# Performance work log

Measured on AMD Instinct MI355X. Metric: run time of the kernel, lower is better.

Reference implementation:

```python
import jax, jax.numpy as jnp
import numpy as np

B, C_HR, C_LR, HH, WH, HL, WL = 2, 256, 256, 128, 128, 64, 64
CC = 64            # compressed channels
LK, HK, EK = 5, 3, 3
GROUPS, LW, SCALE = 4, 3, 2


def conv2d(x, w, b, pad, dilation=1):
    out = jax.lax.conv_general_dilated(
        x, w, (1, 1), [(pad, pad), (pad, pad)],
        rhs_dilation=(dilation, dilation),
        dimension_numbers=('NCHW', 'OIHW', 'NCHW'))
    return out + b[None, :, None, None]


def unfold(x, k, dilation=1):
    # torch F.unfold with padding=(k//2)*dilation -> [B,C,k*k,H,W], row-major kernel order
    pad = (k // 2) * dilation
    Bb, C, H, W = x.shape
    xp = jnp.pad(x, ((0, 0), (0, 0), (pad, pad), (pad, pad)))
    patches = [xp[:, :, i * dilation:i * dilation + H, j * dilation:j * dilation + W]
               for i in range(k) for j in range(k)]
    return jnp.stack(patches, axis=2)


def kernel_normalizer(mask, k, hamming):
    n, c, h, w = mask.shape
    mc = c // (k * k)
    m = jax.nn.softmax(mask.reshape(n, mc, k * k, h, w), axis=2)
    m = m.reshape(n, mc, k, k, h, w) * hamming[None, None, :, :, None, None]
    m = m / jnp.sum(m, axis=(2, 3), keepdims=True)
    return m.reshape(n, c, h, w)


def carafe(feat, mask, k, scale):
    # mmcv CARAFE with group=1: mask at output resolution [B,k*k,H*s,W*s]
    Bb, C, H, W = feat.shape
    unf = unfold(feat, k)  # [B,C,k2,H,W]
    if scale == 1:
        return jnp.einsum('bckhw,bkhw->bchw', unf, mask)
    m = mask.reshape(Bb, k * k, H, scale, W, scale)
    out = jnp.einsum('bckhw,bkhpwq->bchpwq', unf, m)
    return out.reshape(Bb, C, H * scale, W * scale)


def group_norm(x, gamma, beta, groups, eps=1e-5):
    Bb, C, H, W = x.shape
    xg = x.reshape(Bb, groups, -1)
    mu = xg.mean(-1, keepdims=True)
    var = xg.var(-1, keepdims=True)
    xn = ((xg - mu) * jax.lax.rsqrt(var + eps)).reshape(Bb, C, H, W)
    return xn * gamma[None, :, None, None] + beta[None, :, None, None]


def compute_similarity(x, k=LW, dilation=2):
    unf = unfold(x, k, dilation)  # [B,C,k2,H,W]
    c = k * k // 2
    center = unf[:, :, c:c + 1]
    eps = 1e-8
    num = jnp.sum(center * unf, axis=1)
    den = (jnp.maximum(jnp.linalg.norm(center, axis=1), eps)
           * jnp.maximum(jnp.linalg.norm(unf, axis=1), eps))
    sim = num / den  # [B,k2,H,W]
    return jnp.concatenate([sim[:, :c], sim[:, c + 1:]], axis=1)


def pixel_shuffle(x, r):
    Bb, C, H, W = x.shape
    x = x.reshape(Bb, C // (r * r), r, r, H, W)
    return x.transpose(0, 1, 4, 2, 5, 3).reshape(Bb, C // (r * r), H * r, W * r)


def pixel_unshuffle(x, r):
    Bb, C, H, W = x.shape
    x = x.reshape(Bb, C, H // r, r, W // r, r)
    return x.transpose(0, 1, 3, 5, 2, 4).reshape(Bb, C * r * r, H // r, W // r)


def grid_sample_border(x, grid):
    # bilinear, padding_mode='border', align_corners=False; grid [N,Hg,Wg,2] (x,y)
    N, C, H, W = x.shape
    gx = jnp.clip((grid[..., 0] + 1.0) * W * 0.5 - 0.5, 0.0, W - 1.0)
    gy = jnp.clip((grid[..., 1] + 1.0) * H * 0.5 - 0.5, 0.0, H - 1.0)
    x0 = jnp.floor(gx); y0 = jnp.floor(gy)
    tx = (gx - x0)[:, None]; ty = (gy - y0)[:, None]
    x0i = x0.astype(jnp.int32); y0i = y0.astype(jnp.int32)
    x1i = jnp.minimum(x0i + 1, W - 1); y1i = jnp.minimum(y0i + 1, H - 1)
    g = jax.vmap(lambda img, yi, xi: img[:, yi, xi])
    v00 = g(x, y0i, x0i); v01 = g(x, y0i, x1i)
    v10 = g(x, y1i, x0i); v11 = g(x, y1i, x1i)
    return (v00 * (1 - tx) * (1 - ty) + v01 * tx * (1 - ty)
            + v10 * (1 - tx) * ty + v11 * tx * ty)


def init_pos():
    h = jnp.arange((-SCALE + 1) / 2, (SCALE - 1) / 2 + 1) / SCALE  # [-0.25, 0.25]
    t = jnp.stack(jnp.meshgrid(h, h, indexing='ij'))
    t = jnp.transpose(t, (0, 2, 1))
    return jnp.tile(t, (1, GROUPS, 1)).reshape(1, -1, 1, 1).astype(jnp.float32)


def dysampler(hr_x, lr_x, feat, gn_hr_w, gn_hr_b, gn_lr_w, gn_lr_b,
              w_off, b_off, w_hoff, b_hoff, w_ds, b_ds, w_hds, b_hds):
    hr_x = group_norm(hr_x, gn_hr_w, gn_hr_b, CC // 8)
    lr_x = group_norm(lr_x, gn_lr_w, gn_lr_b, CC // 8)
    hr_sim = compute_similarity(hr_x)
    lr_sim = compute_similarity(lr_x)
    pad = EK // 2
    off = conv2d(lr_sim, w_off, b_off, pad) + pixel_unshuffle(conv2d(hr_sim, w_hoff, b_hoff, pad), SCALE)
    ds = conv2d(lr_x, w_ds, b_ds, pad) + pixel_unshuffle(conv2d(hr_x, w_hds, b_hds, pad), SCALE)
    offset = off * jax.nn.sigmoid(ds) + init_pos()  # [B, 2*G*s^2, Hl, Wl]
    Bb, _, H, W = offset.shape
    off5 = offset.reshape(Bb, 2, -1, H, W)
    cw = jnp.arange(W, dtype=offset.dtype) + 0.5
    ch = jnp.arange(H, dtype=offset.dtype) + 0.5
    base = jnp.stack([jnp.broadcast_to(cw[None, :], (H, W)),
                      jnp.broadcast_to(ch[:, None], (H, W))])  # [2,H,W] (x,y)
    norm = jnp.array([W, H], offset.dtype).reshape(1, 2, 1, 1, 1)
    coords = 2.0 * (base[None, :, None] + off5) / norm - 1.0  # [B,2,G*s^2,H,W]
    coords = pixel_shuffle(coords.reshape(Bb, -1, H, W), SCALE)  # [B,2*G,sH,sW]
    coords = (coords.reshape(Bb, 2, GROUPS, SCALE * H, SCALE * W)
              .transpose(0, 2, 3, 4, 1)
              .reshape(Bb * GROUPS, SCALE * H, SCALE * W, 2))
    xs = feat.reshape(Bb * GROUPS, -1, feat.shape[-2], feat.shape[-1])
    out = grid_sample_border(xs, coords)
    return out.reshape(Bb, -1, SCALE * H, SCALE * W)


def setup_inputs() -> dict:
    key = jax.random.key(0)
    ks = jax.random.split(key, 16)
    r = lambda i, shape, s=0.05: jax.random.normal(ks[i], shape, jnp.float32) * s
    LC2, HC2 = LK * LK, HK * HK
    SIMC = LW * LW - 1
    OC = 2 * GROUPS * SCALE * SCALE
    OCH = 2 * GROUPS
    return {
        'hr_feat': jax.random.normal(ks[0], (B, C_HR, HH, WH), jnp.float32),
        'lr_feat': jax.random.normal(ks[1], (B, C_LR, HL, WL), jnp.float32),
        'w_hr_comp': r(2, (CC, C_HR, 1, 1)), 'b_hr_comp': r(3, (CC,)),
        'w_lr_comp': r(4, (CC, C_LR, 1, 1)), 'b_lr_comp': r(5, (CC,)),
        'w_enc': r(6, (LC2, CC, EK, EK), 0.01), 'b_enc': r(7, (LC2,), 0.01),
        'w_enc2': r(8, (HC2, CC, EK, EK), 0.01), 'b_enc2': r(9, (HC2,), 0.01),
        'gn_hr_w': jnp.ones((CC,), jnp.float32), 'gn_hr_b': jnp.zeros((CC,), jnp.float32),
        'gn_lr_w': jnp.ones((CC,), jnp.float32), 'gn_lr_b': jnp.zeros((CC,), jnp.float32),
        'w_off': r(10, (OC, SIMC, EK, EK), 0.01), 'b_off': jnp.zeros((OC,), jnp.float32),
        'w_hoff': r(11, (OCH, SIMC, EK, EK), 0.01), 'b_hoff': jnp.zeros((OCH,), jnp.float32),
        'w_ds': r(12, (OC, CC, EK, EK), 0.01), 'b_ds': jnp.zeros((OC,), jnp.float32),
        'w_hds': r(13, (OCH, CC, EK, EK), 0.01), 'b_hds': jnp.zeros((OCH,), jnp.float32),
    }


def reference(hr_feat, lr_feat, w_hr_comp, b_hr_comp, w_lr_comp, b_lr_comp,
              w_enc, b_enc, w_enc2, b_enc2, gn_hr_w, gn_hr_b, gn_lr_w, gn_lr_b,
              w_off, b_off, w_hoff, b_hoff, w_ds, b_ds, w_hds, b_hds):
    ham_lo = jnp.asarray(np.outer(np.hamming(LK), np.hamming(LK)), jnp.float32)
    ham_hi = jnp.asarray(np.outer(np.hamming(HK), np.hamming(HK)), jnp.float32)
    epad = EK // 2
    ch = conv2d(hr_feat, w_hr_comp, b_hr_comp, 0)
    cl = conv2d(lr_feat, w_lr_comp, b_lr_comp, 0)
    # semi_conv + comp_feat_upsample + use_high_pass path
    mask_hr_hr = conv2d(ch, w_enc2, b_enc2, epad)
    mh_init = kernel_normalizer(mask_hr_hr, HK, ham_hi)
    ch = 2.0 * ch - carafe(ch, mh_init, HK, 1)
    mask_lr_hr = conv2d(ch, w_enc, b_enc, epad)
    ml_init = kernel_normalizer(mask_lr_hr, LK, ham_lo)
    mask_lr_lr = carafe(conv2d(cl, w_enc, b_enc, epad), ml_init, LK, 2)
    mask_lr = mask_lr_hr + mask_lr_lr
    ml_init2 = kernel_normalizer(mask_lr, LK, ham_lo)
    mask_hr_lr = carafe(conv2d(cl, w_enc2, b_enc2, epad), ml_init2, LK, 2)
    mask_hr = mask_hr_hr + mask_hr_lr
    mask_lr_n = kernel_normalizer(mask_lr, LK, ham_lo)
    lr_up = carafe(lr_feat, mask_lr_n, LK, 2)
    mask_hr_n = kernel_normalizer(mask_hr, HK, ham_hi)
    hr_out = 2.0 * hr_feat - carafe(hr_feat, mask_hr_n, HK, 1)  # hr_residual
    lr_out = dysampler(ch, cl, lr_up, gn_hr_w, gn_hr_b, gn_lr_w, gn_lr_b,
                       w_off, b_off, w_hoff, b_hoff, w_ds, b_ds, w_hds, b_hds)
    return mask_lr_n, hr_out, lr_out
```

## Files before the change

### kernel.cpp

```cpp
#include <hip/hip_runtime.h>
#include <hip/hip_bf16.h>

typedef __hip_bfloat16 bf16;
#define TPB 256

__device__ __forceinline__ float toF(float v){ return v; }
__device__ __forceinline__ float toF(bf16 v){ return __bfloat162float(v); }
__device__ __forceinline__ float bfu(unsigned short u){
    unsigned int x = ((unsigned int)u) << 16;
    return __uint_as_float(x);
}
template<typename T> __device__ __forceinline__ void stT(T* p, long i, float v);
template<> __device__ __forceinline__ void stT<float>(float* p, long i, float v){ p[i] = v; }
template<> __device__ __forceinline__ void stT<bf16>(bf16* p, long i, float v){ p[i] = __float2bfloat16(v); }

__device__ __forceinline__ void st4bf(bf16* p, const float* a){
    bf16 t0 = __float2bfloat16(a[0]);
    bf16 t1 = __float2bfloat16(a[1]);
    bf16 t2 = __float2bfloat16(a[2]);
    bf16 t3 = __float2bfloat16(a[3]);
    ushort4 pk;
    pk.x = *(unsigned short*)&t0;
    pk.y = *(unsigned short*)&t1;
    pk.z = *(unsigned short*)&t2;
    pk.w = *(unsigned short*)&t3;
    *(ushort4*)p = pk;
}

static inline int nblk(long n){ return (int)((n + TPB - 1) / TPB); }

__global__ void k_detect(const void* hr, int n, int* flag, float* stat)
{
    if (threadIdx.x < 64) stat[threadIdx.x] = 0.f;
    const unsigned short* u = (const unsigned short*)hr;
    int nan = 0, oz = 0, ot = 0;
    for (int i = threadIdx.x; i < n; i += TPB) {
        unsigned short a = u[i] & 0x7FFF;
        if (a >= 0x7F80) nan++;
        if (i & 1) { ot++; if (a == 0) oz++; }
    }
    __shared__ int s1[TPB], s2[TPB], s3[TPB];
    s1[threadIdx.x] = nan; s2[threadIdx.x] = oz; s3[threadIdx.x] = ot;
    __syncthreads();
    if (threadIdx.x == 0) {
        int a = 0, b = 0, c = 0;
        for (int i = 0; i < TPB; i++) { a += s1[i]; b += s2[i]; c += s3[i]; }
        *flag = (a >= 6 || (long)b * 10 >= (long)c * 9) ? 1 : 0;
    }
}

#define P_W_HRC 0
#define P_B_HRC 16384
#define P_W_LRC 16448
#define P_B_LRC 32832
#define P_W_ENC 32896
#define P_B_ENC 47296
#define P_W_ENC2 47321
#define P_B_ENC2 52505
#define P_GNHW 52514
#define P_GNHB 52578
#define P_GNLW 52642
#define P_GNLB 52706
#define P_W_OFF 52770
#define P_B_OFF 55074
#define P_W_HOFF 55106
#define P_B_HOFF 55682
#define P_W_DS 55690
#define P_B_DS 74122
#define P_W_HDS 74154
#define P_B_HDS 78762
#define P_TOT 78770

__constant__ int c_segsz[20]  = {16384,64,16384,64,14400,25,5184,9,64,64,64,64,2304,32,576,8,18432,32,4608,8};
__constant__ int c_segbase[20]= {P_W_HRC,P_B_HRC,P_W_LRC,P_B_LRC,P_W_ENC,P_B_ENC,P_W_ENC2,P_B_ENC2,
                                 P_GNHW,P_GNHB,P_GNLW,P_GNLB,P_W_OFF,P_B_OFF,P_W_HOFF,P_B_HOFF,
                                 P_W_DS,P_B_DS,P_W_HDS,P_B_HDS};
__constant__ int c_segcin[20] = {256,0,256,0, 64,0, 64,0, 0,0,0,0, 8,0, 8,0, 64,0, 64,0};
__constant__ int c_segcout[20]= { 64,0, 64,0, 25,0,  9,0, 0,0,0,0,32,0, 8,0, 32,0,  8,0};
__constant__ int c_segtap[20] = {  1,0,  1,0,  9,0,  9,0, 0,0,0,0, 9,0, 9,0,  9,0,  9,0};

__global__ void k_prep(const void* p0,const void* p1,const void* p2,const void* p3,
                       const void* p4,const void* p5,const void* p6,const void* p7,
                       const void* p8,const void* p9,const void* p10,const void* p11,
                       const void* p12,const void* p13,const void* p14,const void* p15,
                       const void* p16,const void* p17,const void* p18,const void* p19,
                       float* dst, const int* flag)
{
    int idx = blockIdx.x * TPB + threadIdx.x;
    if (idx >= P_TOT) return;
    int s = 0, off = idx;
    while (off >= c_segsz[s]) { off -= c_segsz[s]; s++; }
    const void* sp;
    switch (s) {
        case 0: sp=p0; break;  case 1: sp=p1; break;  case 2: sp=p2; break;  case 3: sp=p3; break;
        case 4: sp=p4; break;  case 5: sp=p5; break;  case 6: sp=p6; break;  case 7: sp=p7; break;
        case 8: sp=p8; break;  case 9: sp=p9; break;  case 10: sp=p10; break; case 11: sp=p11; break;
        case 12: sp=p12; break; case 13: sp=p13; break; case 14: sp=p14; break; case 15: sp=p15; break;
        case 16: sp=p16; break; case 17: sp=p17; break; case 18: sp=p18; break; default: sp=p19; break;
    }
    float v = (*flag) ? ((const float*)sp)[off] : toF(((const bf16*)sp)[off]);
    int doff = off;
    int cin = c_segcin[s];
    if (cin) {
        int t = c_segtap[s], cout = c_segcout[s];
        int co = off / (cin * t);
        int r  = off % (cin * t);
        int ci = r / t, k = r % t;
        doff = (ci * cout + co) * t + k;
    }
    dst[c_segbase[s] + doff] = v;
}

template<typename T>
__device__ void transpLR_body(const T* __restrict__ x, bf16* __restrict__ xT, int Bn)
{
    __shared__ float tile[64][65];
    int bid = blockIdx.x;
    int pg = bid & 63;
    int cg = (bid >> 6) & 3;
    int b  = bid >> 8;
    int tid = threadIdx.x;
    int tr = tid >> 6, tc = tid & 63;
    for (int i = 0; i < 16; i++) {
        int c = tr + i * 4;
        tile[c][tc] = toF(x[(((long)(b * 256 + cg * 64 + c)) << 12) + (pg << 6) + tc]);
    }
    __syncthreads();
    for (int i = 0; i < 16; i++) {
        int p = tr + i * 4;
        xT[((((long)b << 12) + (pg << 6) + p) << 8) + (cg << 6) + tc] = __float2bfloat16(tile[tc][p]);
    }
}
__global__ void k_transpLR(const void* x, bf16* xT, int Bn, const int* flag)
{
    if (*flag) transpLR_body<float>((const float*)x, xT, Bn);
    else       transpLR_body<bf16 >((const bf16*)x,  xT, Bn);
}

__global__ void k_carafe5T(const bf16* __restrict__ featT, const float* __restrict__ mask,
                           bf16* __restrict__ outT, int Bn)
{
    int lane = threadIdx.x & 63;
    int nwg = gridDim.x;
    int bid = blockIdx.x;
    int swz = (nwg & 7) ? bid : ((bid & 7) * (nwg >> 3) + (bid >> 3));
    int wid = (swz << 2) | (threadIdx.x >> 6);
    wid = __builtin_amdgcn_readfirstlane(wid);
    if (wid >= Bn * 4096) return;
    int ipix = wid & 4095;
    int b    = wid >> 12;
    int h = ipix >> 6, w = ipix & 63;
    const bf16*  fb = featT + (((long)b << 12) << 8) + (lane << 2);
    const float* mb = mask + (((long)b * 25) << 14) + (h << 8) + (w << 1);
    float a00[4], a01[4], a10[4], a11[4];
    #pragma unroll
    for (int t = 0; t < 4; t++) { a00[t]=0.f; a01[t]=0.f; a10[t]=0.f; a11[t]=0.f; }
    #pragma unroll
    for (int k = 0; k < 25; k++) {
        const int i = k / 5, j = k % 5;
        int yy = h + i - 2, xx = w + j - 2;
        bool v = (yy >= 0 && yy < 64 && xx >= 0 && xx < 64);
        int yc = v ? yy : 0, xc = v ? xx : 0;
        ushort4 u = *(const ushort4*)(fb + ((long)((yc << 6) + xc) << 8));
        float2 mr0 = *(const float2*)(mb + ((long)k << 14));
        float2 mr1 = *(const float2*)(mb + ((long)k << 14) + 128);
        float m00 = v ? mr0.x : 0.f, m01 = v ? mr0.y : 0.f;
        float m10 = v ? mr1.x : 0.f, m11 = v ? mr1.y : 0.f;
        float f0 = bfu(u.x), f1 = bfu(u.y), f2 = bfu(u.z), f3 = bfu(u.w);
        a00[0] += f0*m00; a00[1] += f1*m00; a00[2] += f2*m00; a00[3] += f3*m00;
        a01[0] += f0*m01; a01[1] += f1*m01; a01[2] += f2*m01; a01[3] += f3*m01;
        a10[0] += f0*m10; a10[1] += f1*m10; a10[2] += f2*m10; a10[3] += f3*m10;
        a11[0] += f0*m11; a11[1] += f1*m11; a11[2] += f2*m11; a11[3] += f3*m11;
    }
    bf16* op = outT + (((long)(b << 14) + (h << 8) + (w << 1)) << 8) + (lane << 2);
    st4bf(op, a00);
    st4bf(op + 256, a01);
    st4bf(op + (128 << 8), a10);
    st4bf(op + (128 << 8) + 256, a11);
}

template<int COUT>
__global__ void k_conv3x3p(const float* __restrict__ x, const float* __restrict__ wf,
                           float* __restrict__ pbuf, int Bn, int CIN, int H, int W, int CS)
{
    int HW = H * W;
    int idx = blockIdx.x * TPB + threadIdx.x;
    if (idx >= Bn * HW) return;
    int chunk = blockIdx.y;
    int pix = idx % HW, b = idx / HW;
    int wx = pix % W, hy = pix / W;
    int off[9]; float msk[9];
    #pragma unroll
    for (int i = 0; i < 3; i++) {
        int yy = hy + i - 1; bool vy = (yy >= 0 && yy < H); int yc = vy ? yy : hy;
        #pragma unroll
        for (int j = 0; j < 3; j++) {
            int xx = wx + j - 1; bool v = vy && (xx >= 0 && xx < W);
            int xc = (xx >= 0 && xx < W) ? xx : wx;
            off[i*3+j] = yc * W + xc; msk[i*3+j] = v ? 1.f : 0.f;
        }
    }
    float acc[COUT];
    #pragma unroll
    for (int co = 0; co < COUT; co++) acc[co] = 0.f;
    int c0 = chunk * CS;
    const float* xb = x + ((long)b * CIN + c0) * HW;
    const float* wb = wf + (long)c0 * COUT * 9;
    #pragma unroll 2
    for (int ci = 0; ci < CS; ci++) {
        const float* xc = xb + (long)ci * HW;
        float t[9];
        #pragma unroll
        for (int k = 0; k < 9; k++) t[k] = xc[off[k]] * msk[k];
        const float* wr = wb + (long)ci * COUT * 9;
        #pragma unroll
        for (int co = 0; co < COUT; co++) {
            const float* wp = wr + co * 9;
            acc[co] += t[0]*wp[0] + t[1]*wp[1] + t[2]*wp[2] + t[3]*wp[3] + t[4]*wp[4]
                     + t[5]*wp[5] + t[6]*wp[6] + t[7]*wp[7] + t[8]*wp[8];
        }
    }
    long pb = ((long)chunk * Bn + b) * COUT * (long)HW + pix;
    #pragma unroll
    for (int co = 0; co < COUT; co++) pbuf[pb + (long)co * HW] = acc[co];
}

__global__ void k_convr(const float* __restrict__ pbuf, const float* __restrict__ bias,
                        float* __restrict__ out, int Bn, int COUT, int HW, int nChunk)
{
    long idx = (long)blockIdx.x * TPB + threadIdx.x;
    if (idx >= (long)Bn * COUT * HW) return;
    int pix = idx % HW;
    int co  = (idx / HW) % COUT;
    int b   = idx / ((long)HW * COUT);
    float v = bias[co];
    for (int ch = 0; ch < nChunk; ch++)
        v += pbuf[(((long)ch * Bn + b) * COUT + co) * HW + pix];
    out[idx] = v;
}

template<typename T, int CG>
__device__ void conv1x1_body(const T* __restrict__ x, const float* __restrict__ wf,
                             const float* __restrict__ bias, float* __restrict__ out,
                             int Bn, int CIN, int HW)
{
    constexpr int NG = 64 / CG;
    int nwg = gridDim.x;
    int bid = blockIdx.x;
    int lid = (nwg & 7) ? bid : ((bid & 7) * (nwg >> 3) + (bid >> 3));
    int grp = lid % NG;
    int pixblk = lid / NG;
    int idx = pixblk * TPB + threadIdx.x;
    if (idx >= Bn * HW) return;
    int pix = idx % HW, b = idx / HW;
    const T* xp = x + (long)b * CIN * HW + pix;
    const float* wb = wf + grp * CG;
    float acc[CG];
    #pragma unroll
    for (int c = 0; c < CG; c++) acc[c] = 0.f;
    #pragma unroll 4
    for (int ci = 0; ci < CIN; ci++) {
        float v = toF(xp[(long)ci * HW]);
        const float* wr = wb + ci * 64;
        #pragma unroll
        for (int c = 0; c < CG; c++) acc[c] += v * wr[c];
    }
    long ob = ((long)b * 64 + grp * CG) * HW + pix;
    #pragma unroll
    for (int c = 0; c < CG; c++) out[ob + (long)c * HW] = acc[c] + bias[grp * CG + c];
}
template<int CG>
__global__ void k_conv1x1(const void* x, const float* wf, const float* bias, float* out,
                          int Bn, int CIN, int HW, const int* flag)
{
    if (*flag) conv1x1_body<float, CG>((const float*)x, wf, bias, out, Bn, CIN, HW);
    else       conv1x1_body<bf16, CG>((const bf16*)x,  wf, bias, out, Bn, CIN, HW);
}

template<int K, typename OT>
__device__ void knorm_body(const float* __restrict__ mask, float* __restrict__ out,
                           OT* __restrict__ outb, int B, int H, int W)
{
    const int K2 = K * K;
    int HWi = H * W;
    int idx = blockIdx.x * TPB + threadIdx.x;
    if (idx >= B * HWi) return;
    int pix = idx % HWi;
    int b   = idx / HWi;
    long HW = (long)HWi;
    long base = (long)b * K2 * HW + pix;
    float v[K2];
    float m = -1e30f;
    for (int k = 0; k < K2; k++) { v[k] = mask[base + k*HW]; m = fmaxf(m, v[k]); }
    float s2 = 0.f;
    for (int k = 0; k < K2; k++) {
        int i = k / K, j = k % K;
        float hi = (K == 3) ? ((i==1)?1.f:0.08f) : ((i==2)?1.f:((i==1||i==3)?0.54f:0.08f));
        float hj = (K == 3) ? ((j==1)?1.f:0.08f) : ((j==2)?1.f:((j==1||j==3)?0.54f:0.08f));
        v[k] = expf(v[k] - m) * hi * hj;
        s2 += v[k];
    }
    float inv = 1.f / s2;
    for (int k = 0; k < K2; k++) {
        float r = v[k] * inv;
        out[base + k*HW] = r;
        if (outb) stT<OT>(outb, base + k*HW, r);
    }
}
template<int K>
__global__ void k_knorm(const float* mask, float* out, void* outb, int B, int H, int W, const int* flag)
{
    if (*flag) knorm_body<K, float>(mask, out, (float*)outb, B, H, W);
    else       knorm_body<K, bf16>(mask, out, (bf16*)outb, B, H, W);
}

template<typename TF, typename TO, int NC>
__device__ void carafe3c_body(const TF* __restrict__ feat, const float* __restrict__ mask,
                              TO* __restrict__ out, int Bn)
{
    constexpr int CH = NC / 8;
    int idx = blockIdx.x * TPB + threadIdx.x;
    if (idx >= Bn * CH * 16384) return;
    int px = idx & 16383;
    int cc = (idx >> 14) % CH;
    int b  = (idx >> 14) / CH;
    int wx = px & 127, hy = px >> 7;
    float mk[9]; int off[9];
    #pragma unroll
    for (int i = 0; i < 3; i++) {
        int yy = hy + i - 1; bool vy = (yy >= 0 && yy < 128); int yc = vy ? yy : hy;
        #pragma unroll
        for (int j = 0; j < 3; j++) {
            int xx = wx + j - 1; bool v = vy && (xx >= 0 && xx < 128);
            int xc = (xx >= 0 && xx < 128) ? xx : wx;
            int k = i*3 + j;
            float m = mask[(((long)b*9 + k) << 14) + px];
            mk[k] = v ? m : 0.f;
            off[k] = (yc << 7) + xc;
        }
    }
    long base = ((long)(b * NC + cc * 8) << 14);
    for (int c = 0; c < 8; c++) {
        const TF* fp = feat + base + ((long)c << 14);
        float ctr = 0.f, acc = 0.f;
        #pragma unroll
        for (int k = 0; k < 9; k++) {
            float v = toF(fp[off[k]]);
            if (k == 4) ctr = v;
            acc += v * mk[k];
        }
        stT<TO>(out, base + ((long)c << 14) + px, 2.f * ctr - acc);
    }
}
__global__ void k_carafe3c_ws(const float* feat, const float* mask, float* out, int Bn)
{
    carafe3c_body<float, float, 64>(feat, mask, out, Bn);
}
__global__ void k_carafe3c_io(const void* feat, const float* mask, void* out, long outOff,
                              int Bn, const int* flag)
{
    if (*flag) carafe3c_body<float, float, 256>((const float*)feat, mask, (float*)out + outOff, Bn);
    else       carafe3c_body<bf16, bf16, 256>((const bf16*)feat, mask, (bf16*)out + outOff, Bn);
}

template<typename TF, typename TO, bool ADD, int CG>
__device__ void carafe5_body(const TF* __restrict__ feat, const float* __restrict__ mask,
                             const float* __restrict__ add, TO* __restrict__ out,
                             int Bn, int C)
{
    int ng = C / CG;
    int idx = blockIdx.x * TPB + threadIdx.x;
    if (idx >= Bn * ng * 16384) return;
    int px = idx & 16383;
    int gi = (idx >> 14) % ng;
    int b  = (idx >> 14) / ng;
    int X = px & 127, Y = px >> 7;
    int h = Y >> 1, w = X >> 1;
    float mk[25]; int off[25];
    const float* mb = mask + (((long)b * 25) << 14) + px;
    #pragma unroll
    for (int i = 0; i < 5; i++) {
        int yy = h + i - 2; bool vy = (yy >= 0 && yy < 64); int yc = vy ? yy : 0;
        #pragma unroll
        for (int j = 0; j < 5; j++) {
            int xx = w + j - 2; bool v = vy && (xx >= 0 && xx < 64);
            int xc = (xx >= 0 && xx < 64) ? xx : 0;
            int k = i*5 + j;
            mk[k] = v ? mb[(long)k << 14] : 0.f;
            off[k] = (yc << 6) + xc;
        }
    }
    int c0 = gi * CG;
    for (int c = 0; c < CG; c++) {
        long fb = ((long)(b * C + c0 + c) << 12);
        long ob = ((long)(b * C + c0 + c) << 14) + px;
        const TF* fp = feat + fb;
        float acc = ADD ? add[ob] : 0.f;
        #pragma unroll
        for (int k = 0; k < 25; k++) acc += toF(fp[off[k]]) * mk[k];
        stT<TO>(out, ob, acc);
    }
}
template<int CG>
__global__ void k_carafe5_ws(const float* feat, const float* mask, const float* add,
                             float* out, int Bn, int C)
{
    carafe5_body<float, float, true, CG>(feat, mask, add, out, Bn, C);
}

__global__ void k_gnstat(const float* __restrict__ x, float* __restrict__ stat, int statBase,
                         int S, int N)
{
    int bid = blockIdx.x;
    int bg = bid / S, sl = bid % S;
    int seg = N / S;
    long base = (long)bg * N + (long)sl * seg;
    float s = 0.f, ss = 0.f;
    for (int i = threadIdx.x; i < seg; i += TPB) {
        float v = x[base + i]; s += v; ss += v * v;
    }
    __shared__ float sh[8];
    for (int off = 32; off; off >>= 1) { s += __shfl_down(s, off); ss += __shfl_down(ss, off); }
    int wave = threadIdx.x >> 6, lane = threadIdx.x & 63;
    if (lane == 0) { sh[wave] = s; sh[4 + wave] = ss; }
    __syncthreads();
    if (threadIdx.x == 0) {
        float ts = 0.f, tss = 0.f;
        for (int i = 0; i < TPB/64; i++) { ts += sh[i]; tss += sh[4 + i]; }
        atomicAdd(&stat[statBase + bg*2], ts);
        atomicAdd(&stat[statBase + bg*2 + 1], tss);
    }
}
__global__ void k_gnapply(const float* __restrict__ x, const float* __restrict__ stat, int statBase,
                          const float* __restrict__ gamma, const float* __restrict__ beta,
                          float* __restrict__ out, int G, int Cg, int HW, int Bn)
{
    long idx = (long)blockIdx.x * TPB + threadIdx.x;
    long total = (long)Bn * G * Cg * HW;
    if (idx >= total) return;
    int bgN = Cg * HW;
    int bg = idx / bgN;
    int r  = idx % bgN;
    int g = bg % G;
    int c = g * Cg + r / HW;
    float s = stat[statBase + bg*2], ss = stat[statBase + bg*2 + 1];
    float mean = s / bgN;
    float inv = rsqrtf(ss / bgN - mean * mean + 1e-5f);
    out[idx] = (x[idx] - mean) * inv * gamma[c] + beta[c];
}

__global__ void k_simp(const float* __restrict__ x, float* __restrict__ pbuf,
                       int Bn, int H, int W, int CS)
{
    int HW = H * W;
    int idx = blockIdx.x * TPB + threadIdx.x;
    if (idx >= Bn * HW) return;
    int chunk = blockIdx.y;
    int pix = idx % HW, b = idx / HW;
    int wx = pix % W, hy = pix / W;
    const int dyv[8] = {-2,-2,-2, 0, 0, 2, 2, 2};
    const int dxv[8] = {-2, 0, 2,-2, 2,-2, 0, 2};
    int off[8]; float msk[8];
    #pragma unroll
    for (int n = 0; n < 8; n++) {
        int yy = hy + dyv[n], xx = wx + dxv[n];
        bool v = (yy >= 0 && yy < H && xx >= 0 && xx < W);
        off[n] = v ? yy * W + xx : pix;
        msk[n] = v ? 1.f : 0.f;
    }
    float dc = 0.f, num[8], dn[8];
    #pragma unroll
    for (int n = 0; n < 8; n++) { num[n] = 0.f; dn[n] = 0.f; }
    const float* xb = x + ((long)b * 64 + chunk * CS) * HW;
    #pragma unroll 2
    for (int ci = 0; ci < CS; ci++) {
        const float* xc = xb + (long)ci * HW;
        float c0 = xc[pix];
        dc += c0 * c0;
        #pragma unroll
        for (int n = 0; n < 8; n++) {
            float v = xc[off[n]] * msk[n];
            num[n] += c0 * v; dn[n] += v * v;
        }
    }
    long base = ((long)chunk * Bn + b) * 17 * (long)HW + pix;
    pbuf[base] = dc;
    #pragma unroll
    for (int n = 0; n < 8; n++) {
        pbuf[base + (long)(1 + n) * HW] = num[n];
        pbuf[base + (long)(9 + n) * HW] = dn[n];
    }
}
__global__ void k_simr(const float* __restrict__ pbuf, float* __restrict__ out,
                       int Bn, int HW, int nChunk)
{
    int idx = blockIdx.x * TPB + threadIdx.x;
    if (idx >= Bn * HW) return;
    int pix = idx % HW, b = idx / HW;
    float dc = 0.f, num[8], dn[8];
    #pragma unroll
    for (int n = 0; n < 8; n++) { num[n] = 0.f; dn[n] = 0.f; }
    for (int ch = 0; ch < nChunk; ch++) {
        long base = ((long)ch * Bn + b) * 17 * (long)HW + pix;
        dc += pbuf[base];
        #pragma unroll
        for (int n = 0; n < 8; n++) {
            num[n] += pbuf[base + (long)(1 + n) * HW];
            dn[n]  += pbuf[base + (long)(9 + n) * HW];
        }
    }
    float nc = fmaxf(sqrtf(dc), 1e-8f);
    #pragma unroll
    for (int n = 0; n < 8; n++)
        out[((long)(b*8 + n)) * HW + pix] = num[n] / (nc * fmaxf(sqrtf(dn[n]), 1e-8f));
}

__global__ void k_offset(const float* __restrict__ lro, const float* __restrict__ hro,
                         const float* __restrict__ lrd, const float* __restrict__ hrd,
                         float* __restrict__ outoff, int B)
{
    int idx = blockIdx.x * TPB + threadIdx.x;
    int total = B * 32 * 64 * 64;
    if (idx >= total) return;
    int wx = idx & 63;
    int hy = (idx >> 6) & 63;
    int o  = (idx >> 12) & 31;
    int b  = idx >> 17;
    int c = o >> 2, p = (o >> 1) & 1, q = o & 1;
    long hridx = ((long)(b*8 + c) * 128 + 2*hy + p) * 128 + 2*wx + q;
    float off = lro[idx] + hro[hridx];
    float dsv = lrd[idx] + hrd[hridx];
    float sg = 1.f / (1.f + expf(-dsv));
    int comp = o >> 4;
    float ip = (comp == 0) ? (q ? 0.25f : -0.25f) : (p ? 0.25f : -0.25f);
    outoff[idx] = off * sg + ip;
}

template<typename OT>
__device__ void gridsampleT_body(const unsigned short* __restrict__ lrupT,
                                 const float* __restrict__ offb, OT* __restrict__ out, int Bn)
{
    int idx = blockIdx.x * TPB + threadIdx.x;
    if (idx >= Bn * 4 * 16384) return;
    int ch0 = blockIdx.y << 5;
    int opix = idx & 16383;
    int g = (idx >> 14) & 3, b = idx >> 16;
    int X = opix & 127, Y = opix >> 7;
    int h = Y >> 1, p = Y & 1, w = X >> 1, q = X & 1;
    int r = g*4 + p*2 + q;
    float offx = offb[((long)(b*32 + r)      << 12) + (h << 6) + w];
    float offy = offb[((long)(b*32 + 16 + r) << 12) + (h << 6) + w];
    float gx = fminf(fmaxf(2.f * (w + 0.5f + offx) - 0.5f, 0.f), 127.f);
    float gy = fminf(fmaxf(2.f * (h + 0.5f + offy) - 0.5f, 0.f), 127.f);
    float x0f = floorf(gx), y0f = floorf(gy);
    float tx = gx - x0f, ty = gy - y0f;
    int x0 = (int)x0f, y0 = (int)y0f;
    int x1 = min(x0 + 1, 127), y1 = min(y0 + 1, 127);
    float w11 = tx * ty, w10 = ty - w11, w01 = tx - w11, w00 = 1.f - tx - ty + w11;
    const unsigned short* base = lrupT + (((long)b << 14) << 8) + (g << 6) + ch0;
    long a00 = ((long)((y0 << 7) + x0)) << 8, a01 = ((long)((y0 << 7) + x1)) << 8;
    long a10 = ((long)((y1 << 7) + x0)) << 8, a11 = ((long)((y1 << 7) + x1)) << 8;
    OT* op = out + ((long)(b * 256 + g * 64 + ch0) << 14) + opix;
    #pragma unroll
    for (int c8 = 0; c8 < 4; c8++) {
        uint4 v00 = *(const uint4*)(base + a00 + c8*8);
        uint4 v01 = *(const uint4*)(base + a01 + c8*8);
        uint4 v10 = *(const uint4*)(base + a10 + c8*8);
        uint4 v11 = *(const uint4*)(base + a11 + c8*8);
        const unsigned short* u00 = (const unsigned short*)&v00;
        const unsigned short* u01 = (const unsigned short*)&v01;
        const unsigned short* u10 = (const unsigned short*)&v10;
        const unsigned short* u11 = (const unsigned short*)&v11;
        #pragma unroll
        for (int t = 0; t < 8; t++) {
            float res = bfu(u00[t])*w00 + bfu(u01[t])*w01 + bfu(u10[t])*w10 + bfu(u11[t])*w11;
            stT<OT>(op, ((long)(c8*8 + t) << 14), res);
        }
    }
}
__global__ void k_gridsampleT(const bf16* lrupT, const float* offb, void* out, long outOff,
                              int Bn, const int* flag)
{
    if (*flag) gridsampleT_body<float>((const unsigned short*)lrupT, offb, (float*)out + outOff, Bn);
    else       gridsampleT_body<bf16 >((const unsigned short*)lrupT, offb, (bf16*)out + outOff, Bn);
}

extern "C" void kernel_launch(void* const* d_in, const int* in_sizes, int n_in,
                              void* d_out, int out_size, void* d_ws, size_t ws_size,
                              hipStream_t stream) {
    const void* hr_feat = d_in[0];
    const void* lr_feat = d_in[1];

    const int B = 2, HH = 128, HL = 64;
    const int HWH = HH*HH, HWL = HL*HL;

    int*   flag = (int*)d_ws;
    float* stat = (float*)d_ws + 4;
    float* P    = (float*)d_ws + 80;
    float* ws   = P + ((P_TOT + 63) & ~63);

    size_t o = 0;
    float* ch0    = ws + o; o += (size_t)B*64*HWH;
    float* clb    = ws + o; o += (size_t)B*64*HWL;
    float* maskHH = ws + o; o += (size_t)B*9*HWH;
    float* tmp9   = ws + o; o += (size_t)B*9*HWH;
    float* chn    = ws + o; o += (size_t)B*64*HWH;
    float* m25a   = ws + o; o += (size_t)B*25*HWH;
    float* m25b   = ws + o; o += (size_t)B*25*HWH;
    float* m25c   = ws + o; o += (size_t)B*25*HWH;
    float* enccl  = ws + o; o += (size_t)B*25*HWL;
    float* enc2cl = ws + o; o += (size_t)B*9*HWL;
    bf16*  lrupT  = (bf16*)(ws + o); o += (size_t)B*256*HWH/2;
    float* lrx    = ws + o; o += (size_t)B*64*HWL;
    float* hrsim  = ws + o; o += (size_t)B*8*HWH;
    float* lrsim  = ws + o; o += (size_t)B*8*HWL;
    float* qhro   = ws + o; o += (size_t)B*8*HWH;
    float* qlro   = ws + o; o += (size_t)B*32*HWL;
    float* qhrd   = ws + o; o += (size_t)B*8*HWH;
    float* qlrd   = ws + o; o += (size_t)B*32*HWL;
    float* offb   = ws + o; o += (size_t)B*32*HWL;
    float* hrx   = ch0;
    float* maskH = m25b;
    float* pbuf3  = tmp9;
    float* pbuf6  = m25b;
    float* pbufL8 = (float*)lrupT;
    float* pbufT  = chn;
    bf16*  lrfT   = (bf16*)hrsim;
    (void)ws_size; (void)n_in;

    long out1Off = (long)B*25*HWH;
    long out2Off = out1Off + (long)B*256*HWH;

    const float* pw_hrc = P + P_W_HRC;  const float* pb_hrc = P + P_B_HRC;
    const float* pw_lrc = P + P_W_LRC;  const float* pb_lrc = P + P_B_LRC;
    const float* pw_enc = P + P_W_ENC;  const float* pb_enc = P + P_B_ENC;
    const float* pw_enc2= P + P_W_ENC2; const float* pb_enc2= P + P_B_ENC2;
    const float* pgnhw  = P + P_GNHW;   const float* pgnhb  = P + P_GNHB;
    const float* pgnlw  = P + P_GNLW;   const float* pgnlb  = P + P_GNLB;
    const float* pw_off = P + P_W_OFF;  const float* pb_off = P + P_B_OFF;
    const float* pw_hoff= P + P_W_HOFF; const float* pb_hoff= P + P_B_HOFF;
    const float* pw_ds  = P + P_W_DS;   const float* pb_ds  = P + P_B_DS;
    const float* pw_hds = P + P_W_HDS;  const float* pb_hds = P + P_B_HDS;

    int nDet = in_sizes[0] < 16384 ? in_sizes[0] : 16384;
    k_detect<<<1, TPB, 0, stream>>>(hr_feat, nDet, flag, stat);
    k_prep<<<nblk(P_TOT), TPB, 0, stream>>>(d_in[2],d_in[3],d_in[4],d_in[5],d_in[6],d_in[7],
        d_in[8],d_in[9],d_in[10],d_in[11],d_in[12],d_in[13],d_in[14],d_in[15],d_in[16],
        d_in[17],d_in[18],d_in[19],d_in[20],d_in[21], P, flag);
    k_transpLR<<<B*4*64, TPB, 0, stream>>>(lr_feat, lrfT, B, flag);

    k_conv1x1<8><<<nblk((long)B*HWH) * 8, TPB, 0, stream>>>(hr_feat, pw_hrc, pb_hrc, ch0, B, 256, HWH, flag);
    k_conv1x1<2><<<nblk((long)B*HWL) * 32, TPB, 0, stream>>>(lr_feat, pw_lrc, pb_lrc, clb, B, 256, HWL, flag);
    k_conv3x3p<9><<<dim3(nblk((long)B*HWH),8), TPB, 0, stream>>>(ch0, pw_enc2, pbuf3, B, 64, HH, HH, 8);
    k_convr<<<nblk((long)B*9*HWH), TPB, 0, stream>>>(pbuf3, pb_enc2, maskHH, B, 9, HWH, 8);
    k_knorm<3><<<nblk((long)B*HWH), TPB, 0, stream>>>(maskHH, tmp9, nullptr, B, HH, HH, flag);
    k_carafe3c_ws<<<nblk((long)B*8*16384), TPB, 0, stream>>>(ch0, tmp9, chn, B);
    k_conv3x3p<25><<<dim3(nblk((long)B*HWH),8), TPB, 0, stream>>>(chn, pw_enc, pbuf6, B, 64, HH, HH, 8);
    k_convr<<<nblk((long)B*25*HWH), TPB, 0, stream>>>(pbuf6, pb_enc, m25a, B, 25, HWH, 8);
    k_knorm<5><<<nblk((long)B*HWH), TPB, 0, stream>>>(m25a, m25b, nullptr, B, HH, HH, flag);
    k_conv3x3p<25><<<dim3(nblk((long)B*HWL),16), TPB, 0, stream>>>(clb, pw_enc, pbufL8, B, 64, HL, HL, 4);
    k_convr<<<nblk((long)B*25*HWL), TPB, 0, stream>>>(pbufL8, pb_enc, enccl, B, 25, HWL, 16);
    k_carafe5_ws<5><<<nblk((long)B*5*16384), TPB, 0, stream>>>(enccl, m25b, m25a, m25c, B, 25);
    k_knorm<5><<<nblk((long)B*HWH), TPB, 0, stream>>>(m25c, m25a, d_out, B, HH, HH, flag);
    k_conv3x3p<9><<<dim3(nblk((long)B*HWL),16), TPB, 0, stream>>>(clb, pw_enc2, pbufL8, B, 64, HL, HL, 4);
    k_convr<<<nblk((long)B*9*HWL), TPB, 0, stream>>>(pbufL8, pb_enc2, enc2cl, B, 9, HWL, 16);
    k_carafe5_ws<3><<<nblk((long)B*3*16384), TPB, 0, stream>>>(enc2cl, m25a, maskHH, maskH, B, 9);
    k_knorm<3><<<nblk((long)B*HWH), TPB, 0, stream>>>(maskH, tmp9, nullptr, B, HH, HH, flag);
    k_carafe3c_io<<<nblk((long)B*32*16384), TPB, 0, stream>>>(hr_feat, tmp9, d_out, out1Off, B, flag);
    k_carafe5T<<<B*4096/4, TPB, 0, stream>>>(lrfT, m25a, lrupT, B);
    k_gnstat<<<16*32, TPB, 0, stream>>>(chn, stat, 0, 32, 8*HWH);
    k_gnapply<<<nblk((long)B*64*HWH), TPB, 0, stream>>>(chn, stat, 0, pgnhw, pgnhb, hrx, 8, 8, HWH, B);
    k_gnstat<<<16*8, TPB, 0, stream>>>(clb, stat, 32, 8, 8*HWL);
    k_gnapply<<<nblk((long)B*64*HWL), TPB, 0, stream>>>(clb, stat, 32, pgnlw, pgnlb, lrx, 8, 8, HWL, B);
    k_simp<<<dim3(nblk((long)B*HWH),8), TPB, 0, stream>>>(hrx, pbufT, B, HH, HH, 8);
    k_simr<<<nblk((long)B*HWH), TPB, 0, stream>>>(pbufT, hrsim, B, HWH, 8);
    k_simp<<<dim3(nblk((long)B*HWL),16), TPB, 0, stream>>>(lrx, pbufT, B, HL, HL, 4);
    k_simr<<<nblk((long)B*HWL), TPB, 0, stream>>>(pbufT, lrsim, B, HWL, 16);
    k_conv3x3p<8><<<dim3(nblk((long)B*HWH),4), TPB, 0, stream>>>(hrsim, pw_hoff, pbufT, B, 8, HH, HH, 2);
    k_convr<<<nblk((long)B*8*HWH), TPB, 0, stream>>>(pbufT, pb_hoff, qhro, B, 8, HWH, 4);
    k_conv3x3p<32><<<dim3(nblk((long)B*HWL),8), TPB, 0, stream>>>(lrsim, pw_off, pbufT, B, 8, HL, HL, 1);
    k_convr<<<nblk((long)B*32*HWL), TPB, 0, stream>>>(pbufT, pb_off, qlro, B, 32, HWL, 8);
    k_conv3x3p<8><<<dim3(nblk((long)B*HWH),8), TPB, 0, stream>>>(hrx, pw_hds, pbufT, B, 64, HH, HH, 8);
    k_convr<<<nblk((long)B*8*HWH), TPB, 0, stream>>>(pbufT, pb_hds, qhrd, B, 8, HWH, 8);
    k_conv3x3p<32><<<dim3(nblk((long)B*HWL),16), TPB, 0, stream>>>(lrx, pw_ds, pbufT, B, 64, HL, HL, 4);
    k_convr<<<nblk((long)B*32*HWL), TPB, 0, stream>>>(pbufT, pb_ds, qlrd, B, 32, HWL, 16);
    k_offset<<<nblk((long)B*32*HWL), TPB, 0, stream>>>(qlro, qhro, qlrd, qhrd, offb, B);
    k_gridsampleT<<<dim3(nblk((long)B*4*HWH),2), TPB, 0, stream>>>(lrupT, offb, d_out, out2Off, B, flag);
}
```

Baseline: 604.3 us.

## Replace split-K 3x3 convs with LDS-tiled fused-bias kernels and tile 1x1 convs

Six 64-input-channel 3x3 convolutions move from a split-channel partial-sum kernel plus a separate reduction kernel to a single kernel. That kernel stages input row tiles with halos in shared memory, splits output channels across blockIdx.y, and adds the bias directly. The 1x1 compression convs now stage 64-channel input slices in shared memory, with each thread computing 16 output channels. This removes the partial-buffer writes and reduce launches, at the cost of fewer parallel blocks and per-thread weight reads from global/scalar memory.

```diff
diff --git a/kernel.cpp b/kernel.cpp
--- a/kernel.cpp
+++ b/kernel.cpp
@@ -239,42 +239,101 @@
     out[idx] = v;
 }
 
-template<typename T, int CG>
-__device__ void conv1x1_body(const T* __restrict__ x, const float* __restrict__ wf,
-                             const float* __restrict__ bias, float* __restrict__ out,
-                             int Bn, int CIN, int HW)
-{
-    constexpr int NG = 64 / CG;
-    int nwg = gridDim.x;
-    int bid = blockIdx.x;
-    int lid = (nwg & 7) ? bid : ((bid & 7) * (nwg >> 3) + (bid >> 3));
-    int grp = lid % NG;
-    int pixblk = lid / NG;
-    int idx = pixblk * TPB + threadIdx.x;
-    if (idx >= Bn * HW) return;
-    int pix = idx % HW, b = idx / HW;
-    const T* xp = x + (long)b * CIN * HW + pix;
-    const float* wb = wf + grp * CG;
+template<int W, int CG>
+__global__ void k_conv3x3f(const float* __restrict__ x, const float* __restrict__ wf,
+                           const float* __restrict__ bias, float* __restrict__ out,
+                           int Bn, int H, int COUT)
+{
+    constexpr int TR = 256 / W;
+    constexpr int WP = W + 2;
+    constexpr int CB = 4;
+    constexpr int NE = CB * (TR + 2) * WP;
+    __shared__ float s[CB][TR + 2][WP];
+    int tile = blockIdx.x;
+    int cog  = blockIdx.y;
+    int rows_g = tile * TR;
+    int b  = rows_g / H;
+    int r0 = rows_g % H;
+    int HW = H * W;
+    int tid = threadIdx.x;
+    int row = tid / W, col = tid % W;
     float acc[CG];
     #pragma unroll
     for (int c = 0; c < CG; c++) acc[c] = 0.f;
-    #pragma unroll 4
-    for (int ci = 0; ci < CIN; ci++) {
-        float v = toF(xp[(long)ci * HW]);
-        const float* wr = wb + ci * 64;
-        #pragma unroll
-        for (int c = 0; c < CG; c++) acc[c] += v * wr[c];
-    }
-    long ob = ((long)b * 64 + grp * CG) * HW + pix;
-    #pragma unroll
-    for (int c = 0; c < CG; c++) out[ob + (long)c * HW] = acc[c] + bias[grp * CG + c];
-}
-template<int CG>
-__global__ void k_conv1x1(const void* x, const float* wf, const float* bias, float* out,
-                          int Bn, int CIN, int HW, const int* flag)
-{
-    if (*flag) conv1x1_body<float, CG>((const float*)x, wf, bias, out, Bn, CIN, HW);
-    else       conv1x1_body<bf16, CG>((const bf16*)x,  wf, bias, out, Bn, CIN, HW);
+    const float* xb = x + (long)b * 64 * HW;
+    for (int c0 = 0; c0 < 64; c0 += CB) {
+        __syncthreads();
+        for (int e = tid; e < NE; e += 256) {
+            int ci  = e / ((TR + 2) * WP);
+            int rem = e % ((TR + 2) * WP);
+            int rr = rem / WP, cc = rem % WP;
+            int gr = r0 - 1 + rr, gc = cc - 1;
+            bool v = (gr >= 0 && gr < H && gc >= 0 && gc < W);
+            s[ci][rr][cc] = v ? xb[(long)(c0 + ci) * HW + gr * W + gc] : 0.f;
+        }
+        __syncthreads();
+        #pragma unroll
+        for (int ci = 0; ci < CB; ci++) {
+            float t0 = s[ci][row  ][col  ], t1 = s[ci][row  ][col+1], t2 = s[ci][row  ][col+2];
+            float t3 = s[ci][row+1][col  ], t4 = s[ci][row+1][col+1], t5 = s[ci][row+1][col+2];
+            float t6 = s[ci][row+2][col  ], t7 = s[ci][row+2][col+1], t8 = s[ci][row+2][col+2];
+            const float* wr = wf + ((long)(c0 + ci) * COUT + cog * CG) * 9;
+            #pragma unroll
+            for (int c = 0; c < CG; c++) {
+                const float* wp = wr + c * 9;
+                acc[c] += t0*wp[0] + t1*wp[1] + t2*wp[2] + t3*wp[3] + t4*wp[4]
+                        + t5*wp[5] + t6*wp[6] + t7*wp[7] + t8*wp[8];
+            }
+        }
+    }
+    int pp = (r0 + row) * W + col;
+    #pragma unroll
+    for (int c = 0; c < CG; c++) {
+        int co = cog * CG + c;
+        out[((long)b * COUT + co) * HW + pp] = acc[c] + bias[co];
+    }
+}
+
+template<typename T>
+__device__ void conv1x1f_body(const T* __restrict__ x, const float* __restrict__ wf,
+                              const float* __restrict__ bias, float* __restrict__ out,
+                              int Bn, int HW)
+{
+    __shared__ float s[64][64];
+    int tile = blockIdx.x;
+    int tid = threadIdx.x;
+    int pix = tid & 63, grp = tid >> 6;
+    int g0 = tile * 64;
+    int b  = g0 / HW, pp0 = g0 % HW;
+    const T* xb = x + (long)b * 256 * HW + pp0;
+    float acc[16];
+    #pragma unroll
+    for (int c = 0; c < 16; c++) acc[c] = 0.f;
+    for (int c0 = 0; c0 < 256; c0 += 64) {
+        __syncthreads();
+        #pragma unroll
+        for (int k = 0; k < 16; k++) {
+            int ci = grp + k * 4;
+            s[ci][pix] = toF(xb[(long)(c0 + ci) * HW + pix]);
+        }
+        __syncthreads();
+        #pragma unroll 8
+        for (int ci = 0; ci < 64; ci++) {
+            float v = s[ci][pix];
+            const float* wr = wf + (c0 + ci) * 64 + grp * 16;
+            #pragma unroll
+            for (int c = 0; c < 16; c++) acc[c] += v * wr[c];
+        }
+    }
+    long ob = ((long)b * 64 + grp * 16) * HW + pp0 + pix;
+    #pragma unroll
+    for (int c = 0; c < 16; c++) out[ob + (long)c * HW] = acc[c] + bias[grp * 16 + c];
+}
+__global__ void k_conv1x1f(const void* x, const float* wf, const float* bias, float* out,
+                           int Bn, int HW, const int* flag)
+{
+    if (*flag) conv1x1f_body<float>((const float*)x, wf, bias, out, Bn, HW);
+    else       conv1x1f_body<bf16 >((const bf16*)x,  wf, bias, out, Bn, HW);
 }
 
 template<int K, typename OT>
@@ -621,9 +680,6 @@
     float* offb   = ws + o; o += (size_t)B*32*HWL;
     float* hrx   = ch0;
     float* maskH = m25b;
-    float* pbuf3  = tmp9;
-    float* pbuf6  = m25b;
-    float* pbufL8 = (float*)lrupT;
     float* pbufT  = chn;
     bf16*  lrfT   = (bf16*)hrsim;
     (void)ws_size; (void)n_in;
@@ -649,21 +705,17 @@
         d_in[17],d_in[18],d_in[19],d_in[20],d_in[21], P, flag);
     k_transpLR<<<B*4*64, TPB, 0, stream>>>(lr_feat, lrfT, B, flag);
 
-    k_conv1x1<8><<<nblk((long)B*HWH) * 8, TPB, 0, stream>>>(hr_feat, pw_hrc, pb_hrc, ch0, B, 256, HWH, flag);
-    k_conv1x1<2><<<nblk((long)B*HWL) * 32, TPB, 0, stream>>>(lr_feat, pw_lrc, pb_lrc, clb, B, 256, HWL, flag);
-    k_conv3x3p<9><<<dim3(nblk((long)B*HWH),8), TPB, 0, stream>>>(ch0, pw_enc2, pbuf3, B, 64, HH, HH, 8);
-    k_convr<<<nblk((long)B*9*HWH), TPB, 0, stream>>>(pbuf3, pb_enc2, maskHH, B, 9, HWH, 8);
+    k_conv1x1f<<<(B*HWH)/64, TPB, 0, stream>>>(hr_feat, pw_hrc, pb_hrc, ch0, B, HWH, flag);
+    k_conv1x1f<<<(B*HWL)/64, TPB, 0, stream>>>(lr_feat, pw_lrc, pb_lrc, clb, B, HWL, flag);
+    k_conv3x3f<128,3><<<dim3(B*HWH/256,3), TPB, 0, stream>>>(ch0, pw_enc2, pb_enc2, maskHH, B, HH, 9);
     k_knorm<3><<<nblk((long)B*HWH), TPB, 0, stream>>>(maskHH, tmp9, nullptr, B, HH, HH, flag);
     k_carafe3c_ws<<<nblk((long)B*8*16384), TPB, 0, stream>>>(ch0, tmp9, chn, B);
-    k_conv3x3p<25><<<dim3(nblk((long)B*HWH),8), TPB, 0, stream>>>(chn, pw_enc, pbuf6, B, 64, HH, HH, 8);
-    k_convr<<<nblk((long)B*25*HWH), TPB, 0, stream>>>(pbuf6, pb_enc, m25a, B, 25, HWH, 8);
+    k_conv3x3f<128,5><<<dim3(B*HWH/256,5), TPB, 0, stream>>>(chn, pw_enc, pb_enc, m25a, B, HH, 25);
     k_knorm<5><<<nblk((long)B*HWH), TPB, 0, stream>>>(m25a, m25b, nullptr, B, HH, HH, flag);
-    k_conv3x3p<25><<<dim3(nblk((long)B*HWL),16), TPB, 0, stream>>>(clb, pw_enc, pbufL8, B, 64, HL, HL, 4);
-    k_convr<<<nblk((long)B*25*HWL), TPB, 0, stream>>>(pbufL8, pb_enc, enccl, B, 25, HWL, 16);
+    k_conv3x3f<64,5><<<dim3(B*HWL/256,5), TPB, 0, stream>>>(clb, pw_enc, pb_enc, enccl, B, HL, 25);
     k_carafe5_ws<5><<<nblk((long)B*5*16384), TPB, 0, stream>>>(enccl, m25b, m25a, m25c, B, 25);
     k_knorm<5><<<nblk((long)B*HWH), TPB, 0, stream>>>(m25c, m25a, d_out, B, HH, HH, flag);
-    k_conv3x3p<9><<<dim3(nblk((long)B*HWL),16), TPB, 0, stream>>>(clb, pw_enc2, pbufL8, B, 64, HL, HL, 4);
-    k_convr<<<nblk((long)B*9*HWL), TPB, 0, stream>>>(pbufL8, pb_enc2, enc2cl, B, 9, HWL, 16);
+    k_conv3x3f<64,3><<<dim3(B*HWL/256,3), TPB, 0, stream>>>(clb, pw_enc2, pb_enc2, enc2cl, B, HL, 9);
     k_carafe5_ws<3><<<nblk((long)B*3*16384), TPB, 0, stream>>>(enc2cl, m25a, maskHH, maskH, B, 9);
     k_knorm<3><<<nblk((long)B*HWH), TPB, 0, stream>>>(maskH, tmp9, nullptr, B, HH, HH, flag);
     k_carafe3c_io<<<nblk((long)B*32*16384), TPB, 0, stream>>>(hr_feat, tmp9, d_out, out1Off, B, flag);
@@ -680,10 +732,8 @@
     k_convr<<<nblk((long)B*8*HWH), TPB, 0, stream>>>(pbufT, pb_hoff, qhro, B, 8, HWH, 4);
     k_conv3x3p<32><<<dim3(nblk((long)B*HWL),8), TPB, 0, stream>>>(lrsim, pw_off, pbufT, B, 8, HL, HL, 1);
     k_convr<<<nblk((long)B*32*HWL), TPB, 0, stream>>>(pbufT, pb_off, qlro, B, 32, HWL, 8);
-    k_conv3x3p<8><<<dim3(nblk((long)B*HWH),8), TPB, 0, stream>>>(hrx, pw_hds, pbufT, B, 64, HH, HH, 8);
-    k_convr<<<nblk((long)B*8*HWH), TPB, 0, stream>>>(pbufT, pb_hds, qhrd, B, 8, HWH, 8);
-    k_conv3x3p<32><<<dim3(nblk((long)B*HWL),16), TPB, 0, stream>>>(lrx, pw_ds, pbufT, B, 64, HL, HL, 4);
-    k_convr<<<nblk((long)B*32*HWL), TPB, 0, stream>>>(pbufT, pb_ds, qlrd, B, 32, HWL, 16);
+    k_conv3x3f<128,2><<<dim3(B*HWH/256,4), TPB, 0, stream>>>(hrx, pw_hds, pb_hds, qhrd, B, HH, 8);
+    k_conv3x3f<64,4><<<dim3(B*HWL/256,8), TPB, 0, stream>>>(lrx, pw_ds, pb_ds, qlrd, B, HL, 32);
     k_offset<<<nblk((long)B*32*HWL), TPB, 0, stream>>>(qlro, qhro, qlrd, qhrd, offb, B);
     k_gridsampleT<<<dim3(nblk((long)B*4*HWH),2), TPB, 0, stream>>>(lrupT, offb, d_out, out2Off, B, flag);
 }
```

New measurement: 839.8 us. 1.39x slower.
